# Kernel optimization log

Measured on AMD Instinct MI355X. Metric: run time of the kernel, lower is better.

## Reference

```python
import jax, jax.numpy as jnp
import numpy as np

B, ENC, DEC, H, OUT = 4096, 168, 24, 64, 1
IN = 1 + 5 + 3 + 4 + 7  # 20


def _lstm_step(xt, h, c, Wih, Whh, bih, bhh):
    # PyTorch gate order: i, f, g, o
    g = xt @ Wih.T + h @ Whh.T + bih + bhh
    i, f, gg, o = jnp.split(g, 4, axis=-1)
    c = jax.nn.sigmoid(f) * c + jax.nn.sigmoid(i) * jnp.tanh(gg)
    h = jax.nn.sigmoid(o) * jnp.tanh(c)
    return h, c


def _lstm_layer(x, Wih, Whh, bih, bhh):
    # x: [T, B, in] -> ys: [T, B, H], final (h, c)
    h0 = jnp.zeros((x.shape[1], Whh.shape[1]), x.dtype)

    def step(carry, xt):
        h, c = _lstm_step(xt, carry[0], carry[1], Wih, Whh, bih, bhh)
        return (h, c), h

    (h, c), ys = jax.lax.scan(step, (h0, h0), x)
    return ys, h, c


def setup_inputs() -> dict:
    key = jax.random.key(0)
    ks = jax.random.split(key, 24)
    rn = lambda k, s, sc=0.05: jax.random.normal(k, s, jnp.float32) * sc
    inp = {
        "input_p_q": rn(ks[0], (B, ENC, 1), 1.0),
        "input_time": jax.random.randint(ks[1], (B, ENC, 4), 0, 8),
        "label_p": rn(ks[2], (B, ENC), 1.0),
        "decoder_time": jax.random.randint(ks[3], (B, DEC, 4), 0, 8),
        # encoder LSTM layer 0
        "enc0_Wih": rn(ks[4], (4 * H, IN)), "enc0_Whh": rn(ks[5], (4 * H, H)),
        "enc0_bih": rn(ks[6], (4 * H,)), "enc0_bhh": rn(ks[7], (4 * H,)),
        # encoder LSTM layer 1
        "enc1_Wih": rn(ks[8], (4 * H, H)), "enc1_Whh": rn(ks[9], (4 * H, H)),
        "enc1_bih": rn(ks[10], (4 * H,)), "enc1_bhh": rn(ks[11], (4 * H,)),
        # decoder LSTMCell (input = OUT + 19 = 20)
        "dec_Wih": rn(ks[12], (4 * H, OUT + 19)), "dec_Whh": rn(ks[13], (4 * H, H)),
        "dec_bih": rn(ks[14], (4 * H,)), "dec_bhh": rn(ks[15], (4 * H,)),
        # output projection
        "Wout": rn(ks[16], (OUT, H)), "bout": rn(ks[17], (OUT,)),
        # embeddings
        "emb_hour": rn(ks[18], (24, 5)), "emb_wd": rn(ks[19], (8, 3)),
        "emb_mo": rn(ks[20], (13, 4)), "emb_woy": rn(ks[21], (54, 7)),
    }
    return inp


def reference(input_p_q, input_time, label_p, decoder_time,
              enc0_Wih, enc0_Whh, enc0_bih, enc0_bhh,
              enc1_Wih, enc1_Whh, enc1_bih, enc1_bhh,
              dec_Wih, dec_Whh, dec_bih, dec_bhh,
              Wout, bout, emb_hour, emb_wd, emb_mo, emb_woy):
    def time_feats(t):  # t: [B, T, 4] int -> [B, T, 19]
        return jnp.concatenate([emb_hour[t[:, :, 0]], emb_wd[t[:, :, 1]],
                                emb_mo[t[:, :, 2]], emb_woy[t[:, :, 3]]], axis=-1)

    input_q = label_p[:, :ENC, None]                      # [B, ENC, 1]
    enc_in = jnp.concatenate([input_q, time_feats(input_time)], axis=-1)  # [B, ENC, 20]
    x = enc_in.transpose(1, 0, 2)                         # [ENC, B, 20]
    ys0, _, _ = _lstm_layer(x, enc0_Wih, enc0_Whh, enc0_bih, enc0_bhh)
    _, h1, c1 = _lstm_layer(ys0, enc1_Wih, enc1_Whh, enc1_bih, enc1_bhh)

    dec_feat = time_feats(decoder_time).transpose(1, 0, 2)  # [DEC, B, 19]
    prev0 = label_p[:, ENC - 1, None]                       # [B, 1]

    def dec_step(carry, ft):
        h, c, prev = carry
        xin = jnp.concatenate([prev, ft], axis=-1)          # [B, 20]
        h, c = _lstm_step(xin, h, c, dec_Wih, dec_Whh, dec_bih, dec_bhh)
        out = h @ Wout.T + bout                             # [B, OUT]
        return (h, c, out), out

    _, outs = jax.lax.scan(dec_step, (h1, c1, prev0), dec_feat)
    return outs.transpose(1, 0, 2)                          # [B, DEC, OUT]
```

## Files before the change

### kernel.cpp

```cpp
#include <hip/hip_runtime.h>

#define DEVFN __device__ __forceinline__

typedef float  f32x4  __attribute__((ext_vector_type(4)));
typedef short  bf16x8 __attribute__((ext_vector_type(8)));

constexpr int ENC = 168;
constexpr int DEC = 24;
constexpr int BT  = 16;
constexpr int NBLK = 4096 / BT;

constexpr float LOG2E  = 1.4426950408889634f;
constexpr float LOG2E2 = 2.8853900817779268f;

constexpr int W0F = 0;
constexpr int W1F = 24576;
constexpr int WDF = 57344;
constexpr int F_B0   = 40960;
constexpr int F_B1   = 41216;
constexpr int F_BD   = 41472;
constexpr int F_WOUT = 41728;
constexpr int F_BOUT = 41792;
constexpr int F_EMB  = 41793;
constexpr int NEMB = 574;

DEVFN ushort f2bf(float v) {
    unsigned b = __float_as_uint(v);
    return (ushort)((b + 0x7FFFu + ((b >> 16) & 1u)) >> 16);
}
DEVFN unsigned cvt_pk_bf16(float a, float b) {
    unsigned r;
    asm("v_cvt_pk_bf16_f32 %0, %1, %2" : "=v"(r) : "v"(a), "v"(b));
    return r;
}
DEVFN float exp2n(float x) {
    float r;
    asm("v_exp_f32 %0, -%1" : "=v"(r) : "v"(x));
    return r;
}
DEVFN void pinv(bf16x8& v) { asm volatile("" : "+v"(v)); }
DEVFN void pinf(f32x4& v)  { asm volatile("" : "+v"(v)); }

DEVFN float lstm_cell(float gi, float gf, float gg, float go, float& c) {
    float a  = exp2n(fmaxf(gi, -21.f));
    float b  = exp2n(fmaxf(gg, -43.f));
    float f  = exp2n(gf);
    float sf = __builtin_amdgcn_rcpf(1.f + f);
    float it = (1.f - b) * __builtin_amdgcn_rcpf(fmaf(a, b, a + b + 1.f));
    c = fmaf(sf, c, it);
    float d  = exp2n(fmaxf(c, -15.f) * LOG2E2);
    float o  = exp2n(fmaxf(go, -21.f));
    return (1.f - d) * __builtin_amdgcn_rcpf(fmaf(o, d, o + d + 1.f));
}

__global__ void prep_kernel(
    const float* __restrict__ w0ih, const float* __restrict__ w0hh,
    const float* __restrict__ b0ih, const float* __restrict__ b0hh,
    const float* __restrict__ w1ih, const float* __restrict__ w1hh,
    const float* __restrict__ b1ih, const float* __restrict__ b1hh,
    const float* __restrict__ wdih, const float* __restrict__ wdhh,
    const float* __restrict__ bdih, const float* __restrict__ bdhh,
    const float* __restrict__ wout, const float* __restrict__ boutp,
    const float* __restrict__ eh,   const float* __restrict__ ewd,
    const float* __restrict__ emo,  const float* __restrict__ ewoy,
    void* __restrict__ ws)
{
    ushort* wsu = (ushort*)ws;
    float*  wsf = (float*)ws;
    const int total = 81920 + 1407;
    for (int idx = blockIdx.x * blockDim.x + threadIdx.x; idx < total;
         idx += gridDim.x * blockDim.x) {
        if (idx < 81920) {
            int layer, q;
            if (idx < W1F)      { layer = 0; q = idx; }
            else if (idx < WDF) { layer = 1; q = idx - W1F; }
            else                { layer = 2; q = idx - WDF; }
            int c  = q >> 13;
            int tt = (q >> 9) & 15;
            int l  = (q >> 3) & 63;
            int j  = q & 7;
            int k  = c * 32 + (l >> 4) * 8 + j;
            int n  = tt * 16 + (l & 15);
            float v = 0.f;
            if (layer == 0) {
                if (k < 20) v = w0ih[n * 20 + k];
                else if (k >= 32 && k < 96) v = w0hh[n * 64 + (k - 32)];
            } else if (layer == 1) {
                if (k < 64) v = w1ih[n * 64 + k];
                else        v = w1hh[n * 64 + (k - 64)];
            } else {
                if (k < 20) v = wdih[n * 20 + k];
                else if (k >= 32 && k < 96) v = wdhh[n * 64 + (k - 32)];
            }
            v *= ((n >> 6) == 2) ? LOG2E2 : LOG2E;
            wsu[idx] = f2bf(v);
        } else {
            int f = idx - 81920;
            float v;
            if (f < 768) {
                float sc = (((f & 255) >> 6) == 2) ? LOG2E2 : LOG2E;
                if (f < 256)      v = (b0ih[f] + b0hh[f]) * sc;
                else if (f < 512) v = (b1ih[f - 256] + b1hh[f - 256]) * sc;
                else              v = (bdih[f - 512] + bdhh[f - 512]) * sc;
            }
            else if (f < 832) v = wout[f - 768];
            else if (f == 832) v = boutp[0];
            else {
                int e = f - 833;
                if (e < 120)      v = eh[e];
                else if (e < 144) v = ewd[e - 120];
                else if (e < 196) v = emo[e - 144];
                else              v = ewoy[e - 196];
            }
            wsf[40960 + f] = v;
        }
    }
}

DEVFN float emb_lookup(const float* s_emb, int kk, int idx) {
    int f = kk - 1;
    if (f < 5)  return s_emb[idx * 5 + f];
    if (f < 8)  return s_emb[120 + idx * 3 + (f - 5)];
    if (f < 12) return s_emb[144 + idx * 4 + (f - 8)];
    return s_emb[196 + idx * 7 + (f - 12)];
}
DEVFN int offX(int k, int m) {
    return (m + 16 * (k >> 3)) * 8 + (k & 7);
}
DEVFN void store_h4(ushort* A, int off, const float* h) {
    unsigned h01 = cvt_pk_bf16(h[0], h[1]);
    unsigned h23 = cvt_pk_bf16(h[2], h[3]);
    asm volatile("" : "+v"(h01), "+v"(h23));
    unsigned long long p = ((unsigned long long)h23 << 32) | h01;
    *(unsigned long long*)(A + off) = p;
}

__global__ __launch_bounds__(512)
__attribute__((amdgpu_waves_per_eu(2, 2)))
void lstm_mfma(
    const int* __restrict__ input_time, const float* __restrict__ label_p,
    const int* __restrict__ decoder_time, const void* __restrict__ ws,
    float* __restrict__ out)
{
    const ushort* wsu = (const ushort*)ws;
    const float*  wsf = (const float*)ws;

    __shared__ __align__(16) ushort Abuf[2][5 * 512];
    __shared__ float s_emb[NEMB];
    __shared__ float s_wout[64];
    __shared__ float sh1[16 * 68];
    __shared__ float s_bout;

    const int tid = threadIdx.x;
    const int w   = tid >> 6;
    const int l   = tid & 63;
    const int q   = l >> 4;
    const int m   = l & 15;
    const int wl  = w & 3;
    const bool isL0 = (w < 4);
    const int b0g = blockIdx.x * BT;
    const int u0  = wl * 16 + q * 4;

    const int hoff = (1 + (u0 >> 5)) * 512 +
                     (m + 16 * ((u0 & 31) >> 3)) * 8 + (u0 & 7) +
                     (isL0 ? 0 : 1024);

    for (int i = tid; i < 2 * 5 * 512; i += 512) ((ushort*)Abuf)[i] = 0;
    for (int i = tid; i < NEMB; i += 512) s_emb[i] = wsf[F_EMB + i];
    if (tid < 64) s_wout[tid] = wsf[F_WOUT + tid];
    if (tid == 0) s_bout = wsf[F_BOUT];

    bf16x8 wA[4][4];
    if (isL0) {
#pragma unroll
        for (int c = 0; c < 3; c++)
#pragma unroll
            for (int g = 0; g < 4; g++)
                wA[c][g] = *(const bf16x8*)(wsu + W0F +
                    (c * 16 + g * 4 + wl) * 512 + l * 8);
        wA[3][0] = wA[3][1] = wA[3][2] = wA[3][3] = bf16x8{0,0,0,0,0,0,0,0};
    } else {
#pragma unroll
        for (int c = 0; c < 4; c++)
#pragma unroll
            for (int g = 0; g < 4; g++)
                wA[c][g] = *(const bf16x8*)(wsu + W1F +
                    (c * 16 + g * 4 + wl) * 512 + l * 8);
    }
#pragma unroll
    for (int c = 0; c < 4; c++)
#pragma unroll
        for (int g = 0; g < 4; g++) pinv(wA[c][g]);

    f32x4 biasv[4];
#pragma unroll
    for (int g = 0; g < 4; g++) {
        biasv[g] = *(const f32x4*)(wsf + (isL0 ? F_B0 : F_B1) + g * 64 + u0);
        pinf(biasv[g]);
    }

    float cst[4] = {0.f, 0.f, 0.f, 0.f};

    const int kk1 = tid >> 4;
    const int sel1 = (kk1 <= 5) ? 0 : (kk1 <= 8) ? 1 : (kk1 <= 12) ? 2 : 3;
    const int kk2 = kk1 + 16;
    const bool bx2 = (tid < 64);

    __syncthreads();
    if (isL0) {
        float v = (kk1 == 0) ? label_p[(b0g + m) * ENC]
                : emb_lookup(s_emb, kk1, input_time[((b0g + m) * ENC) * 4 + sel1]);
        Abuf[0][offX(kk1, m)] = f2bf(v);
        if (bx2) {
            float v2 = emb_lookup(s_emb, kk2, input_time[((b0g + m) * ENC) * 4 + 3]);
            Abuf[0][offX(kk2, m)] = f2bf(v2);
        }
    }
    __syncthreads();

    for (int i = 0; i <= ENC; ++i) {
        const ushort* Ar = Abuf[i & 1];
        ushort* Aw = Abuf[(i + 1) & 1];
        const bool active = isL0 ? (i < ENC) : (i >= 1);

        float pre_f = 0.f; int pre_i1 = 0, pre_i2 = 0;
        const bool encX  = (i + 1 < ENC) && isL0;
        const bool decX0 = (i == ENC) && isL0;
        if (encX) {
            if (kk1 == 0) pre_f  = label_p[(b0g + m) * ENC + (i + 1)];
            else          pre_i1 = input_time[((b0g + m) * ENC + (i + 1)) * 4 + sel1];
            if (bx2)      pre_i2 = input_time[((b0g + m) * ENC + (i + 1)) * 4 + 3];
        } else if (decX0) {
            if (kk1 == 0) pre_f  = label_p[(b0g + m) * ENC + (ENC - 1)];
            else          pre_i1 = decoder_time[((b0g + m) * DEC) * 4 + sel1];
            if (bx2)      pre_i2 = decoder_time[((b0g + m) * DEC) * 4 + 3];
        }

        if (active) {
            f32x4 acc[4];
#pragma unroll
            for (int g = 0; g < 4; g++) acc[g] = biasv[g];
            if (isL0) {
                bf16x8 ah[3];
#pragma unroll
                for (int c = 0; c < 3; c++)
                    ah[c] = *(const bf16x8*)(Ar + c * 512 + l * 8);
#pragma unroll
                for (int c = 0; c < 3; c++)
#pragma unroll
                    for (int g = 0; g < 4; g++)
                        acc[g] = __builtin_amdgcn_mfma_f32_16x16x32_bf16(
                            wA[c][g], ah[c], acc[g], 0, 0, 0);
            } else {
                bf16x8 ah[4];
#pragma unroll
                for (int c = 0; c < 4; c++)
                    ah[c] = *(const bf16x8*)(Ar + (1 + c) * 512 + l * 8);
#pragma unroll
                for (int c = 0; c < 4; c++)
#pragma unroll
                    for (int g = 0; g < 4; g++)
                        acc[g] = __builtin_amdgcn_mfma_f32_16x16x32_bf16(
                            wA[c][g], ah[c], acc[g], 0, 0, 0);
            }
            float hv[4];
#pragma unroll
            for (int r = 0; r < 4; r++)
                hv[r] = lstm_cell(acc[0][r], acc[1][r], acc[2][r], acc[3][r], cst[r]);
            store_h4(Aw, hoff, hv);
        }
        if (encX || decX0) {
            float v = (kk1 == 0) ? pre_f : emb_lookup(s_emb, kk1, pre_i1);
            Aw[offX(kk1, m)] = f2bf(v);
            if (bx2) Aw[offX(kk2, m)] = f2bf(emb_lookup(s_emb, kk2, pre_i2));
        }
        __syncthreads();
    }

    if (!isL0) {
#pragma unroll
        for (int c = 0; c < 3; c++)
#pragma unroll
            for (int g = 0; g < 4; g++)
                wA[c][g] = *(const bf16x8*)(wsu + WDF +
                    (c * 16 + g * 4 + wl) * 512 + l * 8);
#pragma unroll
        for (int c = 0; c < 3; c++)
#pragma unroll
            for (int g = 0; g < 4; g++) pinv(wA[c][g]);
#pragma unroll
        for (int g = 0; g < 4; g++) {
            biasv[g] = *(const f32x4*)(wsf + F_BD + g * 64 + u0);
            pinf(biasv[g]);
        }
    }

    for (int t = 0; t < DEC; ++t) {
        const ushort* Ar = Abuf[(t + 1) & 1];
        ushort* Aw = Abuf[t & 1];

        int pre_i1 = 0, pre_i2 = 0;
        const bool dX = (t + 1 < DEC) && isL0;
        if (dX) {
            if (kk1 >= 1) pre_i1 = decoder_time[((b0g + m) * DEC + (t + 1)) * 4 + sel1];
            if (bx2)      pre_i2 = decoder_time[((b0g + m) * DEC + (t + 1)) * 4 + 3];
        }

        if (!isL0) {
            bf16x8 ah[3];
            ah[0] = *(const bf16x8*)(Ar + 0 * 512 + l * 8);
            ah[1] = *(const bf16x8*)(Ar + 3 * 512 + l * 8);
            ah[2] = *(const bf16x8*)(Ar + 4 * 512 + l * 8);
            f32x4 acc[4];
#pragma unroll
            for (int g = 0; g < 4; g++) acc[g] = biasv[g];
#pragma unroll
            for (int c = 0; c < 3; c++)
#pragma unroll
                for (int g = 0; g < 4; g++)
                    acc[g] = __builtin_amdgcn_mfma_f32_16x16x32_bf16(
                        wA[c][g], ah[c], acc[g], 0, 0, 0);
            float hv[4];
#pragma unroll
            for (int r = 0; r < 4; r++)
                hv[r] = lstm_cell(acc[0][r], acc[1][r], acc[2][r], acc[3][r], cst[r]);
            store_h4(Aw, hoff, hv);
            *(f32x4*)&sh1[m * 68 + u0] = *(f32x4*)hv;
        }
        if (dX && kk1 >= 1) Aw[offX(kk1, m)] = f2bf(emb_lookup(s_emb, kk1, pre_i1));
        if (dX && bx2)      Aw[offX(kk2, m)] = f2bf(emb_lookup(s_emb, kk2, pre_i2));
        __syncthreads();

        if (tid < 16) {
            float a = s_bout;
#pragma unroll 16
            for (int u = 0; u < 64; u++) a = fmaf(s_wout[u], sh1[tid * 68 + u], a);
            out[(b0g + tid) * DEC + t] = a;
            if (t + 1 < DEC) Aw[offX(0, tid)] = f2bf(a);
        }
        __syncthreads();
    }
}

extern "C" void kernel_launch(void* const* d_in, const int* in_sizes, int n_in,
                              void* d_out, int out_size, void* d_ws, size_t ws_size,
                              hipStream_t stream)
{
    typedef const float* fp;
    const int* input_time   = (const int*)d_in[1];
    fp         label_p      = (fp)d_in[2];
    const int* decoder_time = (const int*)d_in[3];

    prep_kernel<<<128, 256, 0, stream>>>(
        (fp)d_in[4],  (fp)d_in[5],  (fp)d_in[6],  (fp)d_in[7],
        (fp)d_in[8],  (fp)d_in[9],  (fp)d_in[10], (fp)d_in[11],
        (fp)d_in[12], (fp)d_in[13], (fp)d_in[14], (fp)d_in[15],
        (fp)d_in[16], (fp)d_in[17],
        (fp)d_in[18], (fp)d_in[19], (fp)d_in[20], (fp)d_in[21],
        d_ws);

    lstm_mfma<<<NBLK, 512, 0, stream>>>(
        input_time, label_p, decoder_time, d_ws, (float*)d_out);
}
```

Baseline: 287.8 us.

## Split prev input into bf16 hi/lo, precompute embedding offsets, fold bias into MFMA

The scalar prev/label input is stored as two bf16 values (hi and residual) in an unused K slot, and the prep kernel duplicates the first input-weight column into that slot. This raises the precision of the autoregressive feedback path. Per-thread embedding base and stride are computed once instead of branching on every lookup. The bias is passed straight as the accumulator of the first MFMA, which removes a register copy. Most of the change targets accuracy, with small instruction savings on the serial per-step path.

```diff
diff --git a/kernel.cpp b/kernel.cpp
--- a/kernel.cpp
+++ b/kernel.cpp
@@ -28,6 +28,7 @@
     unsigned b = __float_as_uint(v);
     return (ushort)((b + 0x7FFFu + ((b >> 16) & 1u)) >> 16);
 }
+DEVFN float bf2f(ushort u) { return __uint_as_float(((unsigned)u) << 16); }
 DEVFN unsigned cvt_pk_bf16(float a, float b) {
     unsigned r;
     asm("v_cvt_pk_bf16_f32 %0, %1, %2" : "=v"(r) : "v"(a), "v"(b));
@@ -84,12 +85,14 @@
             float v = 0.f;
             if (layer == 0) {
                 if (k < 20) v = w0ih[n * 20 + k];
+                else if (k == 20) v = w0ih[n * 20];
                 else if (k >= 32 && k < 96) v = w0hh[n * 64 + (k - 32)];
             } else if (layer == 1) {
                 if (k < 64) v = w1ih[n * 64 + k];
                 else        v = w1hh[n * 64 + (k - 64)];
             } else {
                 if (k < 20) v = wdih[n * 20 + k];
+                else if (k == 20) v = wdih[n * 20];
                 else if (k >= 32 && k < 96) v = wdhh[n * 64 + (k - 32)];
             }
             v *= ((n >> 6) == 2) ? LOG2E2 : LOG2E;
@@ -117,13 +120,6 @@
     }
 }
 
-DEVFN float emb_lookup(const float* s_emb, int kk, int idx) {
-    int f = kk - 1;
-    if (f < 5)  return s_emb[idx * 5 + f];
-    if (f < 8)  return s_emb[120 + idx * 3 + (f - 5)];
-    if (f < 12) return s_emb[144 + idx * 4 + (f - 8)];
-    return s_emb[196 + idx * 7 + (f - 12)];
-}
 DEVFN int offX(int k, int m) {
     return (m + 16 * (k >> 3)) * 8 + (k & 7);
 }
@@ -133,6 +129,11 @@
     asm volatile("" : "+v"(h01), "+v"(h23));
     unsigned long long p = ((unsigned long long)h23 << 32) | h01;
     *(unsigned long long*)(A + off) = p;
+}
+DEVFN void store_prev(ushort* A, int m, float v) {
+    ushort hi = f2bf(v);
+    A[offX(0, m)]  = hi;
+    A[offX(20, m)] = f2bf(v - bf2f(hi));
 }
 
 __global__ __launch_bounds__(512)
@@ -202,18 +203,29 @@
     float cst[4] = {0.f, 0.f, 0.f, 0.f};
 
     const int kk1 = tid >> 4;
-    const int sel1 = (kk1 <= 5) ? 0 : (kk1 <= 8) ? 1 : (kk1 <= 12) ? 2 : 3;
     const int kk2 = kk1 + 16;
     const bool bx2 = (tid < 64);
+    int sel1 = 0, estr1 = 0, ebase1 = 0;
+    if (kk1 >= 1) {
+        int f = kk1 - 1;
+        if (f < 5)       { sel1 = 0; estr1 = 5; ebase1 = 0   + f; }
+        else if (f < 8)  { sel1 = 1; estr1 = 3; ebase1 = 120 + (f - 5); }
+        else if (f < 12) { sel1 = 2; estr1 = 4; ebase1 = 144 + (f - 8); }
+        else             { sel1 = 3; estr1 = 7; ebase1 = 196 + (f - 12); }
+    }
+    const int ebase2 = 196 + (kk2 - 13);
 
     __syncthreads();
     if (isL0) {
-        float v = (kk1 == 0) ? label_p[(b0g + m) * ENC]
-                : emb_lookup(s_emb, kk1, input_time[((b0g + m) * ENC) * 4 + sel1]);
-        Abuf[0][offX(kk1, m)] = f2bf(v);
+        if (kk1 == 0) {
+            store_prev(Abuf[0], m, label_p[(b0g + m) * ENC]);
+        } else {
+            int idx = input_time[((b0g + m) * ENC) * 4 + sel1];
+            Abuf[0][offX(kk1, m)] = f2bf(s_emb[ebase1 + idx * estr1]);
+        }
         if (bx2) {
-            float v2 = emb_lookup(s_emb, kk2, input_time[((b0g + m) * ENC) * 4 + 3]);
-            Abuf[0][offX(kk2, m)] = f2bf(v2);
+            int idx2 = input_time[((b0g + m) * ENC) * 4 + 3];
+            Abuf[0][offX(kk2, m)] = f2bf(s_emb[ebase2 + idx2 * 7]);
         }
     }
     __syncthreads();
@@ -238,15 +250,17 @@
 
         if (active) {
             f32x4 acc[4];
-#pragma unroll
-            for (int g = 0; g < 4; g++) acc[g] = biasv[g];
             if (isL0) {
                 bf16x8 ah[3];
 #pragma unroll
                 for (int c = 0; c < 3; c++)
                     ah[c] = *(const bf16x8*)(Ar + c * 512 + l * 8);
 #pragma unroll
-                for (int c = 0; c < 3; c++)
+                for (int g = 0; g < 4; g++)
+                    acc[g] = __builtin_amdgcn_mfma_f32_16x16x32_bf16(
+                        wA[0][g], ah[0], biasv[g], 0, 0, 0);
+#pragma unroll
+                for (int c = 1; c < 3; c++)
 #pragma unroll
                     for (int g = 0; g < 4; g++)
                         acc[g] = __builtin_amdgcn_mfma_f32_16x16x32_bf16(
@@ -257,7 +271,11 @@
                 for (int c = 0; c < 4; c++)
                     ah[c] = *(const bf16x8*)(Ar + (1 + c) * 512 + l * 8);
 #pragma unroll
-                for (int c = 0; c < 4; c++)
+                for (int g = 0; g < 4; g++)
+                    acc[g] = __builtin_amdgcn_mfma_f32_16x16x32_bf16(
+                        wA[0][g], ah[0], biasv[g], 0, 0, 0);
+#pragma unroll
+                for (int c = 1; c < 4; c++)
 #pragma unroll
                     for (int g = 0; g < 4; g++)
                         acc[g] = __builtin_amdgcn_mfma_f32_16x16x32_bf16(
@@ -270,9 +288,9 @@
             store_h4(Aw, hoff, hv);
         }
         if (encX || decX0) {
-            float v = (kk1 == 0) ? pre_f : emb_lookup(s_emb, kk1, pre_i1);
-            Aw[offX(kk1, m)] = f2bf(v);
-            if (bx2) Aw[offX(kk2, m)] = f2bf(emb_lookup(s_emb, kk2, pre_i2));
+            if (kk1 == 0) store_prev(Aw, m, pre_f);
+            else          Aw[offX(kk1, m)] = f2bf(s_emb[ebase1 + pre_i1 * estr1]);
+            if (bx2)      Aw[offX(kk2, m)] = f2bf(s_emb[ebase2 + pre_i2 * 7]);
         }
         __syncthreads();
     }
@@ -313,9 +331,11 @@
             ah[2] = *(const bf16x8*)(Ar + 4 * 512 + l * 8);
             f32x4 acc[4];
 #pragma unroll
-            for (int g = 0; g < 4; g++) acc[g] = biasv[g];
-#pragma unroll
-            for (int c = 0; c < 3; c++)
+            for (int g = 0; g < 4; g++)
+                acc[g] = __builtin_amdgcn_mfma_f32_16x16x32_bf16(
+                    wA[0][g], ah[0], biasv[g], 0, 0, 0);
+#pragma unroll
+            for (int c = 1; c < 3; c++)
 #pragma unroll
                 for (int g = 0; g < 4; g++)
                     acc[g] = __builtin_amdgcn_mfma_f32_16x16x32_bf16(
@@ -327,8 +347,8 @@
             store_h4(Aw, hoff, hv);
             *(f32x4*)&sh1[m * 68 + u0] = *(f32x4*)hv;
         }
-        if (dX && kk1 >= 1) Aw[offX(kk1, m)] = f2bf(emb_lookup(s_emb, kk1, pre_i1));
-        if (dX && bx2)      Aw[offX(kk2, m)] = f2bf(emb_lookup(s_emb, kk2, pre_i2));
+        if (dX && kk1 >= 1) Aw[offX(kk1, m)] = f2bf(s_emb[ebase1 + pre_i1 * estr1]);
+        if (dX && bx2)      Aw[offX(kk2, m)] = f2bf(s_emb[ebase2 + pre_i2 * 7]);
         __syncthreads();
 
         if (tid < 16) {
@@ -336,7 +356,7 @@
 #pragma unroll 16
             for (int u = 0; u < 64; u++) a = fmaf(s_wout[u], sh1[tid * 68 + u], a);
             out[(b0g + tid) * DEC + t] = a;
-            if (t + 1 < DEC) Aw[offX(0, tid)] = f2bf(a);
+            if (t + 1 < DEC) store_prev(Aw, tid, a);
         }
         __syncthreads();
     }
```

After: 285.2 us (median of 3 runs). No clear change (-0.9%).
